# Performance work log

Measured on AMD Instinct MI355X. Metric: run time of the kernel, lower is better.

The kernel has to match this reference:

```python
import jax, jax.numpy as jnp
import numpy as np

T, D, E, F = 8192, 1024, 8, 3584


def setup_inputs() -> dict:
    key = jax.random.key(0)
    ks = jax.random.split(key, 5)
    scale_in = 1.0 / np.sqrt(D)
    scale_ff = 1.0 / np.sqrt(F)
    return {
        "x": jax.random.normal(ks[0], (T, D), dtype=jnp.float32),
        "w1": jax.random.normal(ks[1], (E, F, D), dtype=jnp.float32) * scale_in,
        "w3": jax.random.normal(ks[2], (E, F, D), dtype=jnp.float32) * scale_in,
        "w2": jax.random.normal(ks[3], (E, D, F), dtype=jnp.float32) * scale_ff,
        "router_logits": jax.random.normal(ks[4], (T, E), dtype=jnp.float32),
        "top_k": 2,
    }


def reference(x, w1, w3, w2, router_logits, top_k):
    # Routing: softmax over experts, keep top-k, renormalize (Mixtral, normalize=True)
    probs = jax.nn.softmax(router_logits, axis=-1)            # [T, E]
    top_vals, top_idx = jax.lax.top_k(probs, top_k)           # [T, k]
    top_vals = top_vals / jnp.sum(top_vals, axis=-1, keepdims=True)
    tokens = jnp.arange(x.shape[0])[:, None]
    weights = jnp.zeros_like(probs).at[tokens, top_idx].set(top_vals)  # [T, E]

    gate = jnp.einsum('td,efd->tef', x, w1)                   # [T, E, F]
    up = jnp.einsum('td,efd->tef', x, w3)                     # [T, E, F]
    h = jax.nn.silu(gate) * up                                # [T, E, F]
    out = jnp.einsum('te,tef,edf->td', weights, h, w2)        # [T, D]
    return out
```

## Files before the change

### kernel.cpp

```cpp
#include <hip/hip_runtime.h>
#include <cstdint>

#define T_TOK 8192
#define D_DIM 1024
#define E_EXP 8
#define F_DIM 3584
#define NROW  (2 * T_TOK)
#define PROWS_PAD 18432
#define MAXTILES 72
#define MAXBANDS 18
#define G1_GRID (MAXBANDS * 112)
#define W2_ELEMS ((long)E_EXP * D_DIM * F_DIM)
#define W2_CVT_BLOCKS ((int)(W2_ELEMS / (512 * 8)))

typedef __attribute__((ext_vector_type(8))) __bf16 bf16x8;
typedef __attribute__((ext_vector_type(4))) float f32x4;

__device__ __forceinline__ void gload16(const void* g, void* l) {
    __builtin_amdgcn_global_load_lds(
        (const __attribute__((address_space(1))) void*)(g),
        (__attribute__((address_space(3))) void*)(l),
        16, 0, 0);
}

__device__ __forceinline__ void cvt8(const float* __restrict__ in, __bf16* __restrict__ out, long i) {
    const float4 f0 = *(const float4*)(in + i);
    const float4 f1 = *(const float4*)(in + i + 4);
    bf16x8 o;
    o[0] = (__bf16)f0.x; o[1] = (__bf16)f0.y; o[2] = (__bf16)f0.z; o[3] = (__bf16)f0.w;
    o[4] = (__bf16)f1.x; o[5] = (__bf16)f1.y; o[6] = (__bf16)f1.z; o[7] = (__bf16)f1.w;
    *(bf16x8*)(out + i) = o;
}

__global__ void cvt_kernel(const float* __restrict__ in, __bf16* __restrict__ out, long n) {
    long i = ((long)blockIdx.x * blockDim.x + threadIdx.x) * 8;
    if (i >= n) return;
    cvt8(in, out, i);
}

__global__ void route_kernel(const float* __restrict__ rl, int* cnt,
                             int* __restrict__ eidx, float* __restrict__ ewgt) {
    int t = blockIdx.x * blockDim.x + threadIdx.x;
    if (t >= T_TOK) return;
    float l[8];
#pragma unroll
    for (int e = 0; e < 8; ++e) l[e] = rl[t * 8 + e];
    int i0 = 0; float v0 = l[0];
    int i1 = -1; float v1 = -1e30f;
#pragma unroll
    for (int e = 1; e < 8; ++e) {
        if (l[e] > v0) { v1 = v0; i1 = i0; v0 = l[e]; i0 = e; }
        else if (l[e] > v1) { v1 = l[e]; i1 = e; }
    }
    float wsec = 1.f / (1.f + __expf(v0 - v1));
    eidx[2 * t] = i0; eidx[2 * t + 1] = i1;
    ewgt[2 * t] = 1.f - wsec; ewgt[2 * t + 1] = wsec;
    atomicAdd(&cnt[i0], 1); atomicAdd(&cnt[i1], 1);
}

__global__ void scan_kernel(const int* __restrict__ cnt, int* __restrict__ pofs) {
    if (threadIdx.x == 0) {
        int a = 0;
        for (int e = 0; e < E_EXP; ++e) { pofs[e] = a; a += (cnt[e] + 255) & ~255; }
        pofs[E_EXP] = a;
    }
}

__global__ void tiles_kernel(const int* __restrict__ pofs, int* __restrict__ tile_e,
                             int* __restrict__ tile_r0, int* __restrict__ meta) {
    if (threadIdx.x == 0) {
        int n = 0;
        for (int e = 0; e < E_EXP; ++e)
            for (int r = pofs[e]; r < pofs[e + 1]; r += 256) {
                tile_e[n] = e; tile_r0[n] = r; ++n;
            }
        meta[0] = n;
    }
}

__global__ void assign_kernel(const int* __restrict__ eidx, const int* __restrict__ pofs,
                              int* cnt2, int* __restrict__ tokOf, int* __restrict__ rowOf) {
    int t = blockIdx.x * blockDim.x + threadIdx.x;
    if (t >= T_TOK) return;
#pragma unroll
    for (int s = 0; s < 2; ++s) {
        int e = eidx[2 * t + s];
        int pos = atomicAdd(&cnt2[e], 1);
        int prow = pofs[e] + pos;
        tokOf[prow] = t;
        rowOf[2 * t + s] = prow;
    }
}

__global__ void gather_kernel(const float* __restrict__ x, const int* __restrict__ tokOf,
                              __bf16* __restrict__ xg) {
    const int idx = blockIdx.x * blockDim.x + threadIdx.x;
    const int pr = idx >> 7;
    const int j = (idx & 127) * 8;
    const int tk = tokOf[pr];
    bf16x8 o = {};
    if (tk >= 0) {
        const float4 f0 = *(const float4*)(x + (long)tk * D_DIM + j);
        const float4 f1 = *(const float4*)(x + (long)tk * D_DIM + j + 4);
        o[0] = (__bf16)f0.x; o[1] = (__bf16)f0.y; o[2] = (__bf16)f0.z; o[3] = (__bf16)f0.w;
        o[4] = (__bf16)f1.x; o[5] = (__bf16)f1.y; o[6] = (__bf16)f1.z; o[7] = (__bf16)f1.w;
    }
    *(bf16x8*)(xg + (long)pr * D_DIM + j) = o;
}

__device__ __forceinline__ int chunk_row(int c) { return ((c >> 7) << 4) | ((c >> 2) & 15); }
__device__ __forceinline__ int chunk_col(int c) {
    return ((c >> 6) & 1) * 32 + (((c & 3) * 8) ^ (((c >> 5) & 1) << 4));
}

template <int NT>
__device__ __forceinline__ void moe_pipeline(
    const __bf16* const (&srcA)[2][2], const __bf16* const (&srcB)[2][2],
    __bf16 (&Ash)[2][2][8192], __bf16 (&Bsh)[2][2][8192],
    int wave, int abase, int wm, int bh, int bsel, f32x4 (&acc)[8][4])
{
    auto stA = [&](int buf, int kt, int h) {
        const long k0 = (long)kt * 64;
        gload16(srcA[h][0] + k0, &Ash[buf][h][(0 * 512 + wave * 64) * 8]);
        gload16(srcA[h][1] + k0, &Ash[buf][h][(1 * 512 + wave * 64) * 8]);
    };
    auto stB = [&](int buf, int kt, int h) {
        const long k0 = (long)kt * 64;
        gload16(srcB[h][0] + k0, &Bsh[buf][h][(0 * 512 + wave * 64) * 8]);
        gload16(srcB[h][1] + k0, &Bsh[buf][h][(1 * 512 + wave * 64) * 8]);
    };

    bf16x8 bfr[4][2];
    bf16x8 afr[4][2];
    bf16x8 afr2[4][2];

#define LD_A4(dst, Ab, h) \
    _Pragma("unroll") for (int j = 0; j < 4; ++j) { \
        dst[j][0] = *(const bf16x8*)((Ab) + ((4*(h)+j) * 2 + 0) * 512); \
        dst[j][1] = *(const bf16x8*)((Ab) + ((4*(h)+j) * 2 + 1) * 512); \
    }

#define LD_B(Bb) \
    _Pragma("unroll") for (int ni = 0; ni < 4; ++ni) { \
        bfr[ni][0] = *(const bf16x8*)((Bb) + ((bsel * 4 + ni) * 2 + 0) * 512); \
        bfr[ni][1] = *(const bf16x8*)((Bb) + ((bsel * 4 + ni) * 2 + 1) * 512); \
    }

#define MFMA_H(h, src) \
    _Pragma("unroll") for (int j = 0; j < 4; ++j) \
        _Pragma("unroll") for (int ni = 0; ni < 4; ++ni) { \
            acc[4*(h)+j][ni] = __builtin_amdgcn_mfma_f32_16x16x32_bf16(src[j][0], bfr[ni][0], acc[4*(h)+j][ni], 0, 0, 0); \
            acc[4*(h)+j][ni] = __builtin_amdgcn_mfma_f32_16x16x32_bf16(src[j][1], bfr[ni][1], acc[4*(h)+j][ni], 0, 0, 0); \
        }

#define PH_OPEN() \
    __builtin_amdgcn_sched_barrier(0); \
    __builtin_amdgcn_s_barrier(); \
    asm volatile("s_waitcnt lgkmcnt(0)" ::: "memory"); \
    __builtin_amdgcn_sched_barrier(0); \
    __builtin_amdgcn_s_setprio(1);

#define PH_CLOSE() \
    __builtin_amdgcn_s_setprio(0); \
    __builtin_amdgcn_sched_barrier(0); \
    __builtin_amdgcn_s_barrier(); \
    __builtin_amdgcn_sched_barrier(0);

#define PH_CLOSE_G(lastf) \
    __builtin_amdgcn_s_setprio(0); \
    __builtin_amdgcn_sched_barrier(0); \
    if (lastf) { asm volatile("s_waitcnt vmcnt(0)" ::: "memory"); } \
    else       { asm volatile("s_waitcnt vmcnt(4)" ::: "memory"); } \
    __builtin_amdgcn_s_barrier(); \
    __builtin_amdgcn_sched_barrier(0);

    stA(0, 0, 0); stA(0, 0, 1); stB(0, 0, 0); stB(0, 0, 1);
    stB(1, 1, 0); stB(1, 1, 1);
    asm volatile("s_waitcnt vmcnt(4)" ::: "memory");
    __builtin_amdgcn_s_barrier();

    const __bf16* AbE = &Ash[0][wm][abase];
    const __bf16* BbE = &Bsh[0][bh][abase];
    const __bf16* AbO = &Ash[1][wm][abase];
    const __bf16* BbO = &Bsh[1][bh][abase];

    for (int it = 0; it < NT / 2; ++it) {
        const int kv = 2 * it + 1;
        const bool last = (it == NT / 2 - 1);
        LD_A4(afr, AbE, 0) LD_B(BbE)
        stA(1, kv, 0); stA(1, kv, 1);
        PH_OPEN()
        MFMA_H(0, afr)
        LD_A4(afr2, AbE, 1)
        PH_CLOSE()
        if (!last) { stB(0, kv + 1, 0); stB(0, kv + 1, 1); }
        PH_OPEN()
        MFMA_H(1, afr2)
        PH_CLOSE_G(last)
        LD_A4(afr, AbO, 0) LD_B(BbO)
        if (!last) { stA(0, kv + 1, 0); stA(0, kv + 1, 1); }
        PH_OPEN()
        MFMA_H(0, afr)
        LD_A4(afr2, AbO, 1)
        PH_CLOSE()
        if (!last) { stB(1, kv + 2, 0); stB(1, kv + 2, 1); }
        PH_OPEN()
        MFMA_H(1, afr2)
        PH_CLOSE_G(last)
    }
#undef LD_A4
#undef LD_B
#undef MFMA_H
#undef PH_OPEN
#undef PH_CLOSE
#undef PH_CLOSE_G
}

__global__ __launch_bounds__(512, 1)
void gemm1_kernel(const __bf16* __restrict__ xg,
                  const __bf16* __restrict__ w1b,
                  const __bf16* __restrict__ w3b,
                  const int* __restrict__ tile_e,
                  const int* __restrict__ tile_r0,
                  const int* __restrict__ meta,
                  __bf16* __restrict__ h,
                  const float* __restrict__ w2src,
                  __bf16* __restrict__ w2dst) {
    const int bid = blockIdx.x;
    if (bid >= G1_GRID) {
        const long i = ((long)(bid - G1_GRID) * 512 + threadIdx.x) * 8;
        if (i < W2_ELEMS) cvt8(w2src, w2dst, i);
        return;
    }
    const int count = meta[0];
    const int bands = (count + 3) >> 2;
    const int live = bands * 112;
    if (bid >= live) return;
    const int w = (bid & 7) * (live >> 3) + (bid >> 3);
    const int q28 = w / 28, r = w % 28;
    const int tile = (q28 >> 2) * 4 + r / 7;
    const int nt = (q28 & 3) * 7 + r % 7;
    if (tile >= count) return;
    const int e = tile_e[tile];
    const int row0 = tile_r0[tile];

    __shared__ __align__(16) __bf16 Ash[2][2][8192];
    __shared__ __align__(16) __bf16 Bsh[2][2][8192];

    const int tid = threadIdx.x;
    const int wave = tid >> 6, lane = tid & 63;
    const int wm = wave >> 2, wn = wave & 3;
    const int fr = lane & 15, fg = lane >> 4;

    const __bf16* srcA[2][2];
    const __bf16* srcB[2][2];
#pragma unroll
    for (int half = 0; half < 2; ++half)
#pragma unroll
        for (int j = 0; j < 2; ++j) {
            const int c = tid + j * 512;
            srcA[half][j] = xg + (long)(row0 + half * 128 + chunk_row(c)) * D_DIM + chunk_col(c);
            const int rb = half * 128 + chunk_row(c);
            const int blk = rb >> 4;
            const int f = nt * 128 + (blk >> 1) * 16 + (rb & 15);
            srcB[half][j] = ((blk & 1) ? w3b : w1b) + ((long)e * F_DIM + f) * D_DIM + chunk_col(c);
        }

    const int abase = fr * 32 + ((fg * 8) ^ ((fr & 8) << 1));
    f32x4 acc[8][4] = {};

    moe_pipeline<16>(srcA, srcB, Ash, Bsh, wave, abase, wm, wn >> 1, wn & 1, acc);

#pragma unroll
    for (int mi = 0; mi < 8; ++mi) {
#pragma unroll
        for (int reg = 0; reg < 4; ++reg) {
            const int lm = wm * 128 + mi * 16 + fg * 4 + reg;
            const long hrow = (long)(row0 + lm) * F_DIM;
#pragma unroll
            for (int b = 0; b < 2; ++b) {
                const float g = acc[mi][2 * b][reg];
                const float u = acc[mi][2 * b + 1][reg];
                const float s = g / (1.f + __expf(-g));
                h[hrow + nt * 128 + (wn * 2 + b) * 16 + fr] = (__bf16)(s * u);
            }
        }
    }
}

__global__ __launch_bounds__(512, 1)
void gemm2_kernel(const __bf16* __restrict__ hb,
                  const __bf16* __restrict__ w2b,
                  const int* __restrict__ tile_e,
                  const int* __restrict__ tile_r0,
                  const int* __restrict__ meta,
                  __bf16* __restrict__ o2p) {
    const int count = meta[0];
    const int bands = (count + 3) >> 2;
    const int live = bands * 32;
    const int bid = blockIdx.x;
    if (bid >= live) return;
    const int w = (bid & 7) * (live >> 3) + (bid >> 3);
    const int band = w >> 5, s = w & 31;
    const int tile = band * 4 + (s >> 3);
    const int nt = s & 3, ks = (s >> 2) & 1;
    if (tile >= count) return;
    const int e = tile_e[tile];
    const int row0 = tile_r0[tile];

    __shared__ __align__(16) __bf16 Ash[2][2][8192];
    __shared__ __align__(16) __bf16 Bsh[2][2][8192];

    const int tid = threadIdx.x;
    const int wave = tid >> 6, lane = tid & 63;
    const int wm = wave >> 2, wn = wave & 3;
    const int fr = lane & 15, fg = lane >> 4;
    const int kofs = ks * (F_DIM / 2);

    const __bf16* srcA[2][2];
    const __bf16* srcB[2][2];
#pragma unroll
    for (int half = 0; half < 2; ++half)
#pragma unroll
        for (int j = 0; j < 2; ++j) {
            const int c = tid + j * 512;
            srcA[half][j] = hb + (long)(row0 + half * 128 + chunk_row(c)) * F_DIM + kofs + chunk_col(c);
            const int rb = half * 128 + chunk_row(c);
            srcB[half][j] = w2b + ((long)e * D_DIM + nt * 256 + rb) * F_DIM + kofs + chunk_col(c);
        }

    const int abase = fr * 32 + ((fg * 8) ^ ((fr & 8) << 1));
    f32x4 acc[8][4] = {};

    moe_pipeline<28>(srcA, srcB, Ash, Bsh, wave, abase, wm, wn >> 1, wn & 1, acc);

    __bf16* ps = o2p + (long)ks * PROWS_PAD * D_DIM;
#pragma unroll
    for (int mi = 0; mi < 8; ++mi) {
#pragma unroll
        for (int reg = 0; reg < 4; ++reg) {
            const int lm = wm * 128 + mi * 16 + fg * 4 + reg;
            const long obase = (long)(row0 + lm) * D_DIM + nt * 256 + wn * 64 + fr;
#pragma unroll
            for (int ni = 0; ni < 4; ++ni)
                ps[obase + ni * 16] = (__bf16)acc[mi][ni][reg];
        }
    }
}

__global__ void combine_kernel(const __bf16* __restrict__ o2p, const int* __restrict__ rowOf,
                               const float* __restrict__ ewgt, float* __restrict__ out) {
    const int idx = blockIdx.x * blockDim.x + threadIdx.x;
    const int t = idx >> 7;
    const int j = (idx & 127) * 8;
    const long r0 = rowOf[2 * t], r1 = rowOf[2 * t + 1];
    const float w0 = ewgt[2 * t], w1 = ewgt[2 * t + 1];
    float r[8] = {0, 0, 0, 0, 0, 0, 0, 0};
#pragma unroll
    for (int s = 0; s < 2; ++s) {
        const bf16x8 a = *(const bf16x8*)(o2p + ((long)s * PROWS_PAD + r0) * D_DIM + j);
        const bf16x8 b = *(const bf16x8*)(o2p + ((long)s * PROWS_PAD + r1) * D_DIM + j);
#pragma unroll
        for (int q = 0; q < 8; ++q) r[q] += w0 * (float)a[q] + w1 * (float)b[q];
    }
    float4* ob = (float4*)(out + (long)t * D_DIM + j);
    ob[0] = make_float4(r[0], r[1], r[2], r[3]);
    ob[1] = make_float4(r[4], r[5], r[6], r[7]);
}

extern "C" void kernel_launch(void* const* d_in, const int* in_sizes, int n_in,
                              void* d_out, int out_size, void* d_ws, size_t ws_size,
                              hipStream_t stream) {
    const float* x  = (const float*)d_in[0];
    const float* w1 = (const float*)d_in[1];
    const float* w3 = (const float*)d_in[2];
    const float* w2 = (const float*)d_in[3];
    const float* rl = (const float*)d_in[4];
    float* out = (float*)d_out;

    char* ws = (char*)d_ws;
    size_t off = 0;
    auto alloc = [&](size_t bytes) {
        void* p = ws + off;
        off += (bytes + 255) & ~(size_t)255;
        return p;
    };
    __bf16* xg   = (__bf16*)alloc((size_t)PROWS_PAD * D_DIM * 2);
    __bf16* w1b  = (__bf16*)alloc((size_t)E_EXP * F_DIM * D_DIM * 2);
    __bf16* w3b  = (__bf16*)alloc((size_t)E_EXP * F_DIM * D_DIM * 2);
    __bf16* hbuf = (__bf16*)alloc((size_t)PROWS_PAD * F_DIM * 2);
    int*   tokOf = (int*)alloc(PROWS_PAD * 4);
    int*   rowOf = (int*)alloc(NROW * 4);
    int*   eidx  = (int*)alloc(NROW * 4);
    float* ewgt  = (float*)alloc(NROW * 4);
    int*   cnt1  = (int*)alloc(64);
    int*   cnt2  = (int*)alloc(64);
    int*   pofs  = (int*)alloc(64);
    int*   tileE = (int*)alloc(MAXTILES * 4 + 64);
    int*   tileR = (int*)alloc(MAXTILES * 4 + 64);
    int*   meta  = (int*)alloc(64);

    const size_t W2B_BYTES = (size_t)W2_ELEMS * 2;
    const size_t front = off;
    const bool fused = (ws_size >= front + W2B_BYTES);
    __bf16* w2b;
    __bf16* o2p;
    if (fused) {
        w2b = (__bf16*)alloc(W2B_BYTES);
        o2p = (__bf16*)ws;
    } else {
        w2b = (__bf16*)ws;
        o2p = (__bf16*)(ws + W2B_BYTES);
    }

    hipMemsetAsync(cnt1, 0, 64, stream);
    hipMemsetAsync(cnt2, 0, 64, stream);
    hipMemsetAsync(tokOf, 0xFF, PROWS_PAD * 4, stream);

    route_kernel<<<T_TOK / 256, 256, 0, stream>>>(rl, cnt1, eidx, ewgt);
    scan_kernel<<<1, 64, 0, stream>>>(cnt1, pofs);
    tiles_kernel<<<1, 64, 0, stream>>>(pofs, tileE, tileR, meta);
    assign_kernel<<<T_TOK / 256, 256, 0, stream>>>(eidx, pofs, cnt2, tokOf, rowOf);
    gather_kernel<<<PROWS_PAD * 128 / 256, 256, 0, stream>>>(x, tokOf, xg);

    {
        const long n = (long)E_EXP * F_DIM * D_DIM;
        const int blks = (int)(n / 8 / 256);
        cvt_kernel<<<blks, 256, 0, stream>>>(w1, w1b, n);
        cvt_kernel<<<blks, 256, 0, stream>>>(w3, w3b, n);
    }

    if (fused) {
        gemm1_kernel<<<G1_GRID + W2_CVT_BLOCKS, 512, 0, stream>>>(
            xg, w1b, w3b, tileE, tileR, meta, hbuf, w2, w2b);
    } else {
        gemm1_kernel<<<G1_GRID, 512, 0, stream>>>(
            xg, w1b, w3b, tileE, tileR, meta, hbuf, w2, w2b);
        const long n = W2_ELEMS;
        cvt_kernel<<<(int)(n / 8 / 256), 256, 0, stream>>>(w2, w2b, n);
    }

    gemm2_kernel<<<MAXBANDS * 32, 512, 0, stream>>>(hbuf, w2b, tileE, tileR, meta, o2p);

    combine_kernel<<<T_TOK * (D_DIM / 8) / 256, 256, 0, stream>>>(o2p, rowOf, ewgt, out);
}
```

Baseline: 654.4 us.

## Drop split-K in gemm2, use K=32 double-buffered pipeline, merge w1/w3 conversion

The second grouped GEMM no longer splits F into two halves that write separate partial bf16 outputs. Each block now covers the full K with a simpler 32-wide double-buffered LDS pipeline, about 64 KB of LDS where it used 128 KB, and launch bounds allow more blocks per CU. The combine kernel then reads one output buffer instead of summing two partials, which cuts its memory traffic. The w1/w3 fp32-to-bf16 conversions are merged into one launch. The cost is half as many gemm2 blocks (288 max instead of 576), and a shallower K step means more barriers per tile.

```diff
diff --git a/kernel.cpp b/kernel.cpp
--- a/kernel.cpp
+++ b/kernel.cpp
@@ -32,10 +32,14 @@
     *(bf16x8*)(out + i) = o;
 }
 
-__global__ void cvt_kernel(const float* __restrict__ in, __bf16* __restrict__ out, long n) {
-    long i = ((long)blockIdx.x * blockDim.x + threadIdx.x) * 8;
-    if (i >= n) return;
-    cvt8(in, out, i);
+__global__ void cvt2_kernel(const float* __restrict__ in0, __bf16* __restrict__ out0,
+                            const float* __restrict__ in1, __bf16* __restrict__ out1,
+                            long n, int nb) {
+    const int b = blockIdx.x;
+    const float* in = (b < nb) ? in0 : in1;
+    __bf16* out = (b < nb) ? out0 : out1;
+    const long i = ((long)(b < nb ? b : b - nb) * blockDim.x + threadIdx.x) * 8;
+    if (i < n) cvt8(in, out, i);
 }
 
 __global__ void route_kernel(const float* __restrict__ rl, int* cnt,
@@ -111,6 +115,11 @@
 __device__ __forceinline__ int chunk_row(int c) { return ((c >> 7) << 4) | ((c >> 2) & 15); }
 __device__ __forceinline__ int chunk_col(int c) {
     return ((c >> 6) & 1) * 32 + (((c & 3) * 8) ^ (((c >> 5) & 1) << 4));
+}
+
+__device__ __forceinline__ int chunk32_row(int c) { return ((c >> 6) << 4) | ((c >> 2) & 15); }
+__device__ __forceinline__ int chunk32_col(int c) {
+    return ((c & 3) ^ (((c >> 5) & 1) << 1)) * 8;
 }
 
 template <int NT>
@@ -288,53 +297,80 @@
     }
 }
 
-__global__ __launch_bounds__(512, 1)
+__global__ __launch_bounds__(512, 4)
 void gemm2_kernel(const __bf16* __restrict__ hb,
                   const __bf16* __restrict__ w2b,
                   const int* __restrict__ tile_e,
                   const int* __restrict__ tile_r0,
                   const int* __restrict__ meta,
-                  __bf16* __restrict__ o2p) {
+                  __bf16* __restrict__ o2) {
     const int count = meta[0];
-    const int bands = (count + 3) >> 2;
-    const int live = bands * 32;
+    const int live = (count * 4 + 7) & ~7;
     const int bid = blockIdx.x;
     if (bid >= live) return;
     const int w = (bid & 7) * (live >> 3) + (bid >> 3);
-    const int band = w >> 5, s = w & 31;
-    const int tile = band * 4 + (s >> 3);
-    const int nt = s & 3, ks = (s >> 2) & 1;
+    const int tile = w >> 2, nt = w & 3;
     if (tile >= count) return;
     const int e = tile_e[tile];
     const int row0 = tile_r0[tile];
 
-    __shared__ __align__(16) __bf16 Ash[2][2][8192];
-    __shared__ __align__(16) __bf16 Bsh[2][2][8192];
+    __shared__ __align__(16) __bf16 Ash[2][8192];
+    __shared__ __align__(16) __bf16 Bsh[2][8192];
 
     const int tid = threadIdx.x;
     const int wave = tid >> 6, lane = tid & 63;
     const int wm = wave >> 2, wn = wave & 3;
     const int fr = lane & 15, fg = lane >> 4;
-    const int kofs = ks * (F_DIM / 2);
-
-    const __bf16* srcA[2][2];
-    const __bf16* srcB[2][2];
-#pragma unroll
-    for (int half = 0; half < 2; ++half)
-#pragma unroll
-        for (int j = 0; j < 2; ++j) {
-            const int c = tid + j * 512;
-            srcA[half][j] = hb + (long)(row0 + half * 128 + chunk_row(c)) * F_DIM + kofs + chunk_col(c);
-            const int rb = half * 128 + chunk_row(c);
-            srcB[half][j] = w2b + ((long)e * D_DIM + nt * 256 + rb) * F_DIM + kofs + chunk_col(c);
-        }
-
-    const int abase = fr * 32 + ((fg * 8) ^ ((fr & 8) << 1));
+
+    const __bf16* srcA[2];
+    const __bf16* srcB[2];
+#pragma unroll
+    for (int j = 0; j < 2; ++j) {
+        const int c = tid + j * 512;
+        srcA[j] = hb + (long)(row0 + chunk32_row(c)) * F_DIM + chunk32_col(c);
+        srcB[j] = w2b + ((long)e * D_DIM + nt * 256 + chunk32_row(c)) * F_DIM + chunk32_col(c);
+    }
+
+    auto stage = [&](int buf, int kt) {
+        const long k0 = (long)kt * 32;
+        gload16(srcA[0] + k0, &Ash[buf][(tid) * 8]);
+        gload16(srcA[1] + k0, &Ash[buf][(tid + 512) * 8]);
+        gload16(srcB[0] + k0, &Bsh[buf][(tid) * 8]);
+        gload16(srcB[1] + k0, &Bsh[buf][(tid + 512) * 8]);
+    };
+
+    const int foff = fr * 32 + ((fg * 8) ^ ((fr & 8) << 1));
     f32x4 acc[8][4] = {};
 
-    moe_pipeline<28>(srcA, srcB, Ash, Bsh, wave, abase, wm, wn >> 1, wn & 1, acc);
-
-    __bf16* ps = o2p + (long)ks * PROWS_PAD * D_DIM;
+    stage(0, 0);
+    const int NT = F_DIM / 32;
+    for (int t = 0; t < NT; ++t) {
+        const int cur = t & 1;
+        __builtin_amdgcn_sched_barrier(0);
+        asm volatile("s_waitcnt vmcnt(0)" ::: "memory");
+        __builtin_amdgcn_s_barrier();
+        __builtin_amdgcn_sched_barrier(0);
+        if (t + 1 < NT) stage(cur ^ 1, t + 1);
+        bf16x8 af[8], bf[4];
+#pragma unroll
+        for (int mi = 0; mi < 8; ++mi)
+            af[mi] = *(const bf16x8*)(&Ash[cur][(wm * 8 + mi) * 512 + foff]);
+#pragma unroll
+        for (int ni = 0; ni < 4; ++ni)
+            bf[ni] = *(const bf16x8*)(&Bsh[cur][(wn * 4 + ni) * 512 + foff]);
+        asm volatile("s_waitcnt lgkmcnt(0)" ::: "memory");
+        __builtin_amdgcn_sched_barrier(0);
+        __builtin_amdgcn_s_setprio(1);
+#pragma unroll
+        for (int mi = 0; mi < 8; ++mi)
+#pragma unroll
+            for (int ni = 0; ni < 4; ++ni)
+                acc[mi][ni] = __builtin_amdgcn_mfma_f32_16x16x32_bf16(af[mi], bf[ni], acc[mi][ni], 0, 0, 0);
+        __builtin_amdgcn_s_setprio(0);
+        __builtin_amdgcn_sched_barrier(0);
+    }
+    asm volatile("s_waitcnt vmcnt(0)" ::: "memory");
+
 #pragma unroll
     for (int mi = 0; mi < 8; ++mi) {
 #pragma unroll
@@ -343,26 +379,23 @@
             const long obase = (long)(row0 + lm) * D_DIM + nt * 256 + wn * 64 + fr;
 #pragma unroll
             for (int ni = 0; ni < 4; ++ni)
-                ps[obase + ni * 16] = (__bf16)acc[mi][ni][reg];
+                o2[obase + ni * 16] = (__bf16)acc[mi][ni][reg];
         }
     }
 }
 
-__global__ void combine_kernel(const __bf16* __restrict__ o2p, const int* __restrict__ rowOf,
+__global__ void combine_kernel(const __bf16* __restrict__ o2, const int* __restrict__ rowOf,
                                const float* __restrict__ ewgt, float* __restrict__ out) {
     const int idx = blockIdx.x * blockDim.x + threadIdx.x;
     const int t = idx >> 7;
     const int j = (idx & 127) * 8;
     const long r0 = rowOf[2 * t], r1 = rowOf[2 * t + 1];
     const float w0 = ewgt[2 * t], w1 = ewgt[2 * t + 1];
-    float r[8] = {0, 0, 0, 0, 0, 0, 0, 0};
-#pragma unroll
-    for (int s = 0; s < 2; ++s) {
-        const bf16x8 a = *(const bf16x8*)(o2p + ((long)s * PROWS_PAD + r0) * D_DIM + j);
-        const bf16x8 b = *(const bf16x8*)(o2p + ((long)s * PROWS_PAD + r1) * D_DIM + j);
-#pragma unroll
-        for (int q = 0; q < 8; ++q) r[q] += w0 * (float)a[q] + w1 * (float)b[q];
-    }
+    const bf16x8 a = *(const bf16x8*)(o2 + r0 * D_DIM + j);
+    const bf16x8 b = *(const bf16x8*)(o2 + r1 * D_DIM + j);
+    float r[8];
+#pragma unroll
+    for (int q = 0; q < 8; ++q) r[q] = w0 * (float)a[q] + w1 * (float)b[q];
     float4* ob = (float4*)(out + (long)t * D_DIM + j);
     ob[0] = make_float4(r[0], r[1], r[2], r[3]);
     ob[1] = make_float4(r[4], r[5], r[6], r[7]);
@@ -404,13 +437,13 @@
     const size_t front = off;
     const bool fused = (ws_size >= front + W2B_BYTES);
     __bf16* w2b;
-    __bf16* o2p;
+    __bf16* o2;
     if (fused) {
         w2b = (__bf16*)alloc(W2B_BYTES);
-        o2p = (__bf16*)ws;
+        o2 = (__bf16*)ws;
     } else {
         w2b = (__bf16*)ws;
-        o2p = (__bf16*)(ws + W2B_BYTES);
+        o2 = (__bf16*)(ws + W2B_BYTES);
     }
 
     hipMemsetAsync(cnt1, 0, 64, stream);
@@ -425,9 +458,8 @@
 
     {
         const long n = (long)E_EXP * F_DIM * D_DIM;
-        const int blks = (int)(n / 8 / 256);
-        cvt_kernel<<<blks, 256, 0, stream>>>(w1, w1b, n);
-        cvt_kernel<<<blks, 256, 0, stream>>>(w3, w3b, n);
+        const int nb = (int)(n / 8 / 256);
+        cvt2_kernel<<<2 * nb, 256, 0, stream>>>(w1, w1b, w3, w3b, n, nb);
     }
 
     if (fused) {
@@ -437,10 +469,10 @@
         gemm1_kernel<<<G1_GRID, 512, 0, stream>>>(
             xg, w1b, w3b, tileE, tileR, meta, hbuf, w2, w2b);
         const long n = W2_ELEMS;
-        cvt_kernel<<<(int)(n / 8 / 256), 256, 0, stream>>>(w2, w2b, n);
-    }
-
-    gemm2_kernel<<<MAXBANDS * 32, 512, 0, stream>>>(hbuf, w2b, tileE, tileR, meta, o2p);
-
-    combine_kernel<<<T_TOK * (D_DIM / 8) / 256, 256, 0, stream>>>(o2p, rowOf, ewgt, out);
-}
+        cvt2_kernel<<<(int)(n / 8 / 256), 256, 0, stream>>>(w2, w2b, w2, w2b, n, (int)(n / 8 / 256));
+    }
+
+    gemm2_kernel<<<MAXTILES * 4, 512, 0, stream>>>(hbuf, w2b, tileE, tileR, meta, o2);
+
+    combine_kernel<<<T_TOK * (D_DIM / 8) / 256, 256, 0, stream>>>(o2, rowOf, ewgt, out);
+}
```

Result: slower. 2.181 ms (+233.3%).
